# Kernel tuning notes

Measured on AMD Instinct MI355X. Metric: run time of the kernel, lower is better.

## Reference

```python
import jax, jax.numpy as jnp
import numpy as np

jax.config.update("jax_enable_x64", True)

N = 100000   # active sparse sites
H = W = 512  # event-camera grid
CIN, CMID, COUT = 64, 384, 64
SHIFT = 16   # shift_n


def setup_inputs() -> dict:
    rng = np.random.default_rng(0)
    # unique active coordinates on the grid (batch index 0)
    flat = rng.permutation(H * W)[:N]
    ys, xs = flat // W, flat % W
    # dense index map with 1-pixel halo; sentinel N = missing neighbor
    idx_map = np.full((H + 2, W + 2), N, dtype=np.int32)
    idx_map[ys + 1, xs + 1] = np.arange(N, dtype=np.int32)
    # 3x3 neighborhood indices per active site, row-major kernel order
    nbr = np.stack([idx_map[ys + 1 + dy, xs + 1 + dx]
                    for dy in (-1, 0, 1) for dx in (-1, 0, 1)], axis=1)

    def ri(lo, hi, shape):
        return jnp.asarray(rng.integers(lo, hi, size=shape), dtype=jnp.float32)

    return {
        "feats": ri(-128, 128, (N, CIN)),      # int8-valued input features
        "w1": ri(-128, 128, (CIN, CMID)),       # 1x1 expand weights
        "b1": ri(-1024, 1024, (CMID,)),
        "s1": ri(1, 16, (CMID,)),
        "w_dw": ri(-128, 128, (9, CMID)),       # 3x3 depthwise weights [k, C]
        "b2": ri(-1024, 1024, (CMID,)),
        "s2": ri(1, 64, (CMID,)),
        "w3": ri(-128, 128, (CMID, COUT)),      # 1x1 project weights
        "b3": ri(-1024, 1024, (COUT,)),
        "s3": ri(1, 16, (COUT,)),
        "neighbor_idx": jnp.asarray(nbr),       # [N, 9] int32, N = sentinel
    }


def _quant(psum, bias, scale, relu):
    # (psum + bias) * scale, add 2^(shift-1), arithmetic >> shift,
    # clamp to int8 range, optional relu. psum values are exact integers.
    t = psum.astype(jnp.int64)
    t = ((t + bias.astype(jnp.int64)) * scale.astype(jnp.int64)
         + (1 << (SHIFT - 1))) >> SHIFT
    y = jnp.clip(t.astype(jnp.float32), -128.0, 127.0)
    return jnp.maximum(y, 0.0) if relu else y


def reference(feats, w1, b1, s1, w_dw, b2, s2, w3, b3, s3, neighbor_idx):
    # 1x1 expand (sparse 1x1 conv == matmul over active sites) + quant + relu
    x1 = _quant(feats @ w1, b1, s1, True)                       # [N, CMID]
    # 3x3 depthwise sparse conv: gather 9 neighbors (zero row for missing)
    pad = jnp.concatenate([x1, jnp.zeros((1, x1.shape[1]), x1.dtype)], axis=0)
    psum2 = jnp.einsum('nkc,kc->nc', pad[neighbor_idx], w_dw)   # [N, CMID]
    x2 = _quant(psum2, b2, s2, True)
    # 1x1 project + quant (linear bottleneck: no relu)
    x3 = _quant(x2 @ w3, b3, s3, False)                          # [N, COUT]
    return x3
```

## Files before the change

### kernel.cpp

```cpp
#include <hip/hip_runtime.h>
#include <stdint.h>

#define N_SITES 100000
#define NPAD    100032
#define CIN 64
#define CMID 384
#define COUT 64
#define SHIFT 16

typedef int   v4i __attribute__((ext_vector_type(4)));
typedef unsigned int v4u __attribute__((ext_vector_type(4)));
typedef float v4f __attribute__((ext_vector_type(4)));

__global__ __launch_bounds__(256) void pack_w(
    const float* __restrict__ w1, const float* __restrict__ w3,
    const float* __restrict__ b1, const float* __restrict__ s1,
    const float* __restrict__ b2, const float* __restrict__ s2,
    const float* __restrict__ b3, const float* __restrict__ s3,
    const float* __restrict__ wdw,
    int8_t* __restrict__ w1p, int8_t* __restrict__ w3p,
    int* __restrict__ q1, int* __restrict__ q3,
    int8_t* __restrict__ wdw8, int* __restrict__ bs2,
    int8_t* __restrict__ x1s)
{
    int o = blockIdx.x * 256 + threadIdx.x;
    if (o < 24 * 64 * 16) {
        int t = o >> 10, l = (o >> 4) & 63, b = o & 15;
        int k = ((l >> 4) << 4) + b;
        int col = t * 16 + (l & 15);
        w1p[o] = (int8_t)__float2int_rn(w1[k * CMID + col]);
    }
    int o3 = o - 24 * 64 * 16;
    if (o3 >= 0 && o3 < 6 * 4 * 64 * 16) {
        int ks = o3 >> 12, t = (o3 >> 10) & 3;
        int l = (o3 >> 4) & 63, b = o3 & 15;
        int k = ks * 64 + ((l >> 4) << 4) + b;
        int col = t * 16 + (l & 15);
        w3p[o3] = (int8_t)__float2int_rn(w3[k * COUT + col]);
    }
    if (o < 9 * CMID)
        wdw8[o] = (int8_t)__float2int_rn(wdw[o]);
    if (o < CMID) {
        q1[o] = __float2int_rn(b1[o]);
        q1[CMID + o] = __float2int_rn(s1[o]);
        int bb = __float2int_rn(b2[o]);
        int ss = __float2int_rn(s2[o]);
        bs2[o] = (bb & 0xFFFF) | (ss << 16);
        x1s[(size_t)N_SITES * CMID + o] = 0;
    }
    if (o < COUT) {
        q3[o] = __float2int_rn(b3[o]);
        q3[COUT + o] = __float2int_rn(s3[o]);
    }
}

__global__ __launch_bounds__(256) void k1_mfma(
    const float* __restrict__ feats, const int8_t* __restrict__ w1p,
    const int* __restrict__ q1, int8_t* __restrict__ x1s)
{
    __shared__ int8_t xt[64 * 400];
    const int lane = threadIdx.x & 63;
    const int wave = threadIdx.x >> 6;
    const int sl = wave * 16 + (lane & 15);
    const int site = blockIdx.x * 64 + sl;
    const int rsite = min(site, N_SITES - 1);
    const int cb = (lane >> 4) << 2;

    v4i b;
    const float* fp = feats + (size_t)rsite * CIN + ((lane >> 4) << 4);
#pragma unroll
    for (int j = 0; j < 4; ++j) {
        const v4f f = *(const v4f*)(fp + 4 * j);
        uint32_t pk = (uint32_t)(__float2int_rn(f[0]) & 255)
                    | ((uint32_t)(__float2int_rn(f[1]) & 255) << 8)
                    | ((uint32_t)(__float2int_rn(f[2]) & 255) << 16)
                    | ((uint32_t)__float2int_rn(f[3]) << 24);
        b[j] = (int)pk;
    }

    const v4i* ap = (const v4i*)w1p + lane;
#pragma unroll
    for (int t = 0; t < 24; ++t) {
        v4i a = ap[t * 64];
        v4i acc = {0, 0, 0, 0};
        acc = __builtin_amdgcn_mfma_i32_16x16x64_i8(a, b, acc, 0, 0, 0);
        const int co = t * 16 + cb;
        const v4i bi = *(const v4i*)(q1 + co);
        const v4i si = *(const v4i*)(q1 + CMID + co);
        uint32_t wrd = 0;
#pragma unroll
        for (int r = 0; r < 4; ++r) {
            int v = ((acc[r] + bi[r]) * si[r] + (1 << (SHIFT - 1))) >> SHIFT;
            v = max(0, min(127, v));
            wrd |= (uint32_t)v << (8 * r);
        }
        *(uint32_t*)(xt + sl * 400 + co) = wrd;
    }
    __syncthreads();

    int8_t* dst = x1s + (size_t)blockIdx.x * 64 * CMID;
#pragma unroll
    for (int it = 0; it < 6; ++it) {
        const int lin = it * 4096 + threadIdx.x * 16;
        const int r = lin / 384;
        const int c = lin - r * 384;
        const v4u val = *(const v4u*)(xt + r * 400 + c);
        if (blockIdx.x * 64 + r < N_SITES)
            *(v4u*)(dst + lin) = val;
    }
}

__global__ __launch_bounds__(768) void k23(
    const int8_t* __restrict__ x1s, const int* __restrict__ nbr,
    const int8_t* __restrict__ wdw8, const int* __restrict__ bs2,
    const int8_t* __restrict__ w3p, const int* __restrict__ q3,
    float* __restrict__ out)
{
    __shared__ int8_t xt[32 * 400];
    __shared__ float  ot[32 * 68];
    const int tid = threadIdx.x;

    {
        const int sl = tid / 24;
        const int c0 = (tid - sl * 24) << 4;
        const int site = blockIdx.x * 32 + sl;

        const int* nb = &nbr[site * 9];
        int idx[9];
#pragma unroll
        for (int k = 0; k < 9; ++k) idx[k] = nb[k];

        v4u V[9];
#pragma unroll
        for (int k = 0; k < 9; ++k) {
            const int off = (idx[k] << 8) + (idx[k] << 7) + c0;
            V[k] = *(const v4u*)(x1s + off);
        }

        int acc[16];
#pragma unroll
        for (int j = 0; j < 16; ++j) acc[j] = 0;

#pragma unroll
        for (int k = 0; k < 9; ++k) {
            const v4u W = *(const v4u*)(wdw8 + k * CMID + c0);
#pragma unroll
            for (int j = 0; j < 4; ++j) {
#pragma unroll
                for (int b = 0; b < 4; ++b) {
                    const int v = (int)(uint8_t)(V[k][j] >> (8 * b));
                    const int w = (int)(int8_t)(W[j] >> (8 * b));
                    acc[j * 4 + b] += v * w;
                }
            }
        }

        const v4i BS0 = *(const v4i*)(bs2 + c0);
        const v4i BS1 = *(const v4i*)(bs2 + c0 + 4);
        const v4i BS2 = *(const v4i*)(bs2 + c0 + 8);
        const v4i BS3 = *(const v4i*)(bs2 + c0 + 12);
        const v4i BS[4] = {BS0, BS1, BS2, BS3};

        v4u outw;
#pragma unroll
        for (int j = 0; j < 4; ++j) {
            uint32_t wrd = 0;
#pragma unroll
            for (int b = 0; b < 4; ++b) {
                const int bsv = BS[j][b];
                const int bb = (bsv << 16) >> 16;
                const int ss = bsv >> 16;
                int t = ((acc[j * 4 + b] + bb) * ss + (1 << (SHIFT - 1))) >> SHIFT;
                t = max(0, min(127, t));
                wrd |= (uint32_t)t << (8 * b);
            }
            outw[j] = wrd;
        }
        *(v4u*)(xt + sl * 400 + c0) = outw;
    }
    __syncthreads();

    const int wv = tid >> 6;
    if (wv < 2) {
        const int lane = tid & 63;
        const int sl2 = wv * 16 + (lane & 15);
        const int cb = (lane >> 4) << 2;
        const int8_t* xrow = xt + sl2 * 400 + ((lane >> 4) << 4);

        v4i acc[4] = {{0,0,0,0},{0,0,0,0},{0,0,0,0},{0,0,0,0}};
#pragma unroll
        for (int ks = 0; ks < 6; ++ks) {
            const v4i bfr = *(const v4i*)(xrow + ks * 64);
#pragma unroll
            for (int t = 0; t < 4; ++t) {
                const v4i afr = *((const v4i*)w3p + (ks * 4 + t) * 64 + lane);
                acc[t] = __builtin_amdgcn_mfma_i32_16x16x64_i8(afr, bfr, acc[t], 0, 0, 0);
            }
        }
#pragma unroll
        for (int t = 0; t < 4; ++t) {
            const int co = t * 16 + cb;
            const v4i bo = *(const v4i*)(q3 + co);
            const v4i so = *(const v4i*)(q3 + COUT + co);
            v4f o;
#pragma unroll
            for (int r = 0; r < 4; ++r) {
                int v = ((acc[t][r] + bo[r]) * so[r] + (1 << (SHIFT - 1))) >> SHIFT;
                v = max(-128, min(127, v));
                o[r] = (float)v;
            }
            *(v4f*)(&ot[sl2 * 68 + co]) = o;
        }
    }
    __syncthreads();

    if (tid < 512) {
        const int lin = tid * 4;
        const int r = lin >> 6;
        const int c = lin & 63;
        const v4f val = *(const v4f*)(&ot[r * 68 + c]);
        *(v4f*)(out + (size_t)blockIdx.x * 32 * COUT + lin) = val;
    }
}

extern "C" void kernel_launch(void* const* d_in, const int* in_sizes, int n_in,
                              void* d_out, int out_size, void* d_ws, size_t ws_size,
                              hipStream_t stream) {
    const float* feats = (const float*)d_in[0];
    const float* w1    = (const float*)d_in[1];
    const float* b1    = (const float*)d_in[2];
    const float* s1    = (const float*)d_in[3];
    const float* wdw   = (const float*)d_in[4];
    const float* b2    = (const float*)d_in[5];
    const float* s2    = (const float*)d_in[6];
    const float* w3    = (const float*)d_in[7];
    const float* b3    = (const float*)d_in[8];
    const float* s3    = (const float*)d_in[9];
    const int*   nbr   = (const int*)d_in[10];
    float* out = (float*)d_out;

    int8_t* x1s   = (int8_t*)d_ws;
    int8_t* w1p   = x1s + (size_t)(NPAD + 64) * CMID;
    int8_t* w3p   = w1p + 24 * 64 * 16;
    int*    q1    = (int*)(w3p + 6 * 4 * 64 * 16);
    int*    q3    = q1 + 2 * CMID;
    int8_t* wdw8  = (int8_t*)(q3 + 2 * COUT);
    int*    bs2   = (int*)(wdw8 + 9 * CMID);

    pack_w<<<192, 256, 0, stream>>>(w1, w3, b1, s1, b2, s2, b3, s3, wdw,
                                    w1p, w3p, q1, q3, wdw8, bs2, x1s);
    k1_mfma<<<NPAD / 64, 256, 0, stream>>>(feats, w1p, q1, x1s);
    k23<<<N_SITES / 32, 768, 0, stream>>>(x1s, nbr, wdw8, bs2, w3p, q3, out);
}
```

Before: 91.01 us.

## Make k23 wave-independent: each wave handles 16 sites end-to-end

Restructures the fused depthwise+projection kernel so every wave owns 16 sites. It loops six times over the depthwise gather and quantize work, then runs its own MFMA projection and writes output directly to global memory. This removes the block-wide __syncthreads, the idle waves during the MFMA phase, and the LDS staging of the output tile. The cost is a serialized gather loop per wave, which may expose memory latency, and uncoalesced 16-byte strided output stores.

```diff
diff --git a/kernel.cpp b/kernel.cpp
--- a/kernel.cpp
+++ b/kernel.cpp
@@ -110,20 +110,25 @@
     }
 }
 
-__global__ __launch_bounds__(768) void k23(
+__global__ __launch_bounds__(256) void k23(
     const int8_t* __restrict__ x1s, const int* __restrict__ nbr,
     const int8_t* __restrict__ wdw8, const int* __restrict__ bs2,
     const int8_t* __restrict__ w3p, const int* __restrict__ q3,
     float* __restrict__ out)
 {
-    __shared__ int8_t xt[32 * 400];
-    __shared__ float  ot[32 * 68];
-    const int tid = threadIdx.x;
-
-    {
-        const int sl = tid / 24;
-        const int c0 = (tid - sl * 24) << 4;
-        const int site = blockIdx.x * 32 + sl;
+    __shared__ int8_t xt[4][16 * 400];
+    const int lane = threadIdx.x & 63;
+    const int wv = threadIdx.x >> 6;
+    const int site0 = (blockIdx.x * 4 + wv) * 16;
+    if (site0 >= N_SITES) return;
+    int8_t* xw = &xt[wv][0];
+
+#pragma unroll 1
+    for (int t = 0; t < 6; ++t) {
+        const int g = t * 64 + lane;
+        const int sl = g / 24;
+        const int c0 = (g - sl * 24) << 4;
+        const int site = site0 + sl;
 
         const int* nb = &nbr[site * 9];
         int idx[9];
@@ -170,22 +175,23 @@
                 const int bsv = BS[j][b];
                 const int bb = (bsv << 16) >> 16;
                 const int ss = bsv >> 16;
-                int t = ((acc[j * 4 + b] + bb) * ss + (1 << (SHIFT - 1))) >> SHIFT;
-                t = max(0, min(127, t));
-                wrd |= (uint32_t)t << (8 * b);
+                int tq = ((acc[j * 4 + b] + bb) * ss + (1 << (SHIFT - 1))) >> SHIFT;
+                tq = max(0, min(127, tq));
+                wrd |= (uint32_t)tq << (8 * b);
             }
             outw[j] = wrd;
         }
-        *(v4u*)(xt + sl * 400 + c0) = outw;
-    }
-    __syncthreads();
-
-    const int wv = tid >> 6;
-    if (wv < 2) {
-        const int lane = tid & 63;
-        const int sl2 = wv * 16 + (lane & 15);
+        *(v4u*)(xw + sl * 400 + c0) = outw;
+    }
+
+    __builtin_amdgcn_wave_barrier();
+    asm volatile("s_waitcnt lgkmcnt(0)" ::: "memory");
+    __builtin_amdgcn_wave_barrier();
+
+    {
+        const int sl2 = lane & 15;
         const int cb = (lane >> 4) << 2;
-        const int8_t* xrow = xt + sl2 * 400 + ((lane >> 4) << 4);
+        const int8_t* xrow = xw + sl2 * 400 + ((lane >> 4) << 4);
 
         v4i acc[4] = {{0,0,0,0},{0,0,0,0},{0,0,0,0},{0,0,0,0}};
 #pragma unroll
@@ -197,6 +203,7 @@
                 acc[t] = __builtin_amdgcn_mfma_i32_16x16x64_i8(afr, bfr, acc[t], 0, 0, 0);
             }
         }
+        float* orow = out + (size_t)(site0 + sl2) * COUT;
 #pragma unroll
         for (int t = 0; t < 4; ++t) {
             const int co = t * 16 + cb;
@@ -209,17 +216,8 @@
                 v = max(-128, min(127, v));
                 o[r] = (float)v;
             }
-            *(v4f*)(&ot[sl2 * 68 + co]) = o;
-        }
-    }
-    __syncthreads();
-
-    if (tid < 512) {
-        const int lin = tid * 4;
-        const int r = lin >> 6;
-        const int c = lin & 63;
-        const v4f val = *(const v4f*)(&ot[r * 68 + c]);
-        *(v4f*)(out + (size_t)blockIdx.x * 32 * COUT + lin) = val;
+            *(v4f*)(orow + co) = o;
+        }
     }
 }
 
@@ -250,5 +248,6 @@
     pack_w<<<192, 256, 0, stream>>>(w1, w3, b1, s1, b2, s2, b3, s3, wdw,
                                     w1p, w3p, q1, q3, wdw8, bs2, x1s);
     k1_mfma<<<NPAD / 64, 256, 0, stream>>>(feats, w1p, q1, x1s);
-    k23<<<N_SITES / 32, 768, 0, stream>>>(x1s, nbr, wdw8, bs2, w3p, q3, out);
-}
+    k23<<<(N_SITES / 16 + 3) / 4, 256, 0, stream>>>(x1s, nbr, wdw8, bs2,
+                                                    w3p, q3, out);
+}
```

Measured after the change: 92.78 us. No clear change (+1.9%).
